# Kernel tuning notes

Hardware: AMD Instinct MI355X
Metric: run time of the kernel (lower is better)

Reference implementation:

```python
import jax, jax.numpy as jnp
import numpy as np

B, S, D, H = 2, 2048, 1024, 16
DH = D // H


def setup_inputs() -> dict:
    key = jax.random.key(0)
    ks = jax.random.split(key, 12)
    f = lambda k, sh: jax.random.normal(k, sh, dtype=jnp.float32)
    inp = {"q": f(ks[0], (B, S, D)), "k": f(ks[1], (B, S, D)), "v": f(ks[2], (B, S, D))}
    scale = 1.0 / np.sqrt(D)
    names = ["q", "k", "v", "o"]
    for i, n in enumerate(names):
        inp["W" + n] = f(ks[3 + i], (D, D)) * scale
        inp["b" + n] = f(ks[7 + i], (D,)) * scale
    # causal mask: True = masked out
    inp["mask"] = jnp.triu(jnp.ones((S, S), dtype=bool), k=1)[None, None]
    return inp


def _rope(x):
    # x: [b, h, s, dh]; non-standard RoPE from AbsPositionEncoding
    s, dh = x.shape[2], x.shape[3]
    inv = jnp.exp(jnp.arange(0, dh, 2, dtype=jnp.float32) * (-(4.0 * jnp.log(jnp.float32(10.0))) / dh))
    pos = jnp.arange(s, dtype=jnp.float32)[:, None]
    sin = jnp.sin(pos * inv)  # [s, dh/2]
    cos = jnp.cos(pos * inv)
    x1 = x[..., 0::2]
    x2 = x[..., 1::2]
    out = jnp.stack([x1 * sin - x2 * cos, -x1 * cos - x2 * sin], axis=-1)
    return out.reshape(x.shape)


def reference(q, k, v, Wq, bq, Wk, bk, Wv, bv, Wo, bo, mask):
    b, s, d = q.shape
    h, dh = H, DH

    def proj(x, W, bias):
        return (x @ W.T + bias).reshape(b, -1, h, dh).transpose(0, 2, 1, 3)

    Q = proj(q, Wq, bq)
    K = proj(k, Wk, bk)
    V = proj(v, Wv, bv)
    PQ = _rope(Q)
    PK = _rope(K)
    # NOTE: source's forward() path applies NO 1/sqrt(dh) scaling
    scores = jnp.einsum('bhqd,bhkd->bhqk', PQ, PK)
    neg = jnp.finfo(scores.dtype).min
    scores = jnp.where(mask, neg, scores)
    p = jax.nn.softmax(scores, axis=-1)
    p = jnp.where(mask, jnp.float32(0.0), p)
    out = jnp.einsum('bhqk,bhkd->bhqd', p, V)
    out = out.transpose(0, 2, 1, 3).reshape(b, s, d)
    return out @ Wo.T + bo
```

## Files before the change

kernel.cpp:

```cpp
#include <hip/hip_runtime.h>
#include <stdint.h>

#define BB 2
#define SS 2048
#define DD 1024
#define HH 16
#define DH 64
#define MM 4096
#define NQT 32

typedef __attribute__((ext_vector_type(8))) short short8;
typedef __attribute__((ext_vector_type(4))) float floatx4;
typedef unsigned short u16;

#define MFMA16(a,b,c) __builtin_amdgcn_mfma_f32_16x16x32_bf16((a),(b),(c),0,0,0)

__device__ __forceinline__ u16 f2bf(float f) {
  unsigned u = __float_as_uint(f);
  u += 0x7fffu + ((u >> 16) & 1u);
  return (u16)(u >> 16);
}

__device__ __forceinline__ void gll16(const void* g, void* l) {
  __builtin_amdgcn_global_load_lds((const __attribute__((address_space(1))) void*)g,
                                   (__attribute__((address_space(3))) void*)l,
                                   16, 0, 0);
}

__global__ __launch_bounds__(256) void sincos_k(float2* __restrict__ tab) {
  const int t = blockIdx.x * 256 + threadIdx.x;
  const int s = t >> 5, j = t & 31;
  const float inv = expf(-(float)j * (0.125f * 2.302585092994046f));
  const float a = (float)s * inv;
  tab[t] = make_float2(sinf(a), cosf(a));
}

__global__ __launch_bounds__(256) void conv_qkv(const float* __restrict__ a, const float* __restrict__ b,
                                                const float* __restrict__ c,
                                                u16* __restrict__ oa, u16* __restrict__ ob, u16* __restrict__ oc) {
  const float* s = blockIdx.y == 0 ? a : (blockIdx.y == 1 ? b : c);
  u16* d = blockIdx.y == 0 ? oa : (blockIdx.y == 1 ? ob : oc);
  const int i = (blockIdx.x * 256 + threadIdx.x) * 4;
  const float4 x = *(const float4*)(s + i);
  ushort4 p; p.x = f2bf(x.x); p.y = f2bf(x.y); p.z = f2bf(x.z); p.w = f2bf(x.w);
  *(ushort4*)(d + i) = p;
}

__global__ __launch_bounds__(256) void conv_w(const float* __restrict__ a, const float* __restrict__ b,
                                              const float* __restrict__ c, const float* __restrict__ d4,
                                              u16* __restrict__ oa, u16* __restrict__ ob,
                                              u16* __restrict__ oc, u16* __restrict__ od) {
  const float* s = blockIdx.y == 0 ? a : (blockIdx.y == 1 ? b : (blockIdx.y == 2 ? c : d4));
  u16* d = blockIdx.y == 0 ? oa : (blockIdx.y == 1 ? ob : (blockIdx.y == 2 ? oc : od));
  const int i = (blockIdx.x * 256 + threadIdx.x) * 4;
  const float4 x = *(const float4*)(s + i);
  ushort4 p; p.x = f2bf(x.x); p.y = f2bf(x.y); p.z = f2bf(x.z); p.w = f2bf(x.w);
  *(ushort4*)(d + i) = p;
}

__device__ __forceinline__ void gemm_body(const u16* __restrict__ A, const u16* __restrict__ Bt,
                                          const float* __restrict__ bias, float* __restrict__ C,
                                          int M, int N, int K, u16* As, u16* Bs) {
  const int tid = threadIdx.x;
  const int w = tid >> 6, l = tid & 63;
  const int lr = l & 15, lq = l >> 4;
  const int m0 = blockIdx.y * 128, n0 = blockIdx.x * 128;
  const int wm = (w >> 1) * 64, wn = (w & 1) * 64;

  floatx4 acc[4][4];
#pragma unroll
  for (int i = 0; i < 4; ++i)
#pragma unroll
    for (int j = 0; j < 4; ++j) acc[i][j] = (floatx4){0.f, 0.f, 0.f, 0.f};

  const int srow = w * 32 + (l >> 2);
  const int scol = (l & 3) * 8;
  const u16* ag = A + (size_t)(m0 + srow) * K + scol;
  const u16* bg = Bt + (size_t)(n0 + srow) * K + scol;
  u16* as0 = &As[w * 1024];
  u16* bs0 = &Bs[w * 1024];

  for (int k0 = 0; k0 < K; k0 += 32) {
    gll16(ag + k0, as0);
    gll16(ag + (size_t)16 * K + k0, as0 + 512);
    gll16(bg + k0, bs0);
    gll16(bg + (size_t)16 * K + k0, bs0 + 512);
    __syncthreads();
    short8 af[4], bfv[4];
#pragma unroll
    for (int i = 0; i < 4; ++i) af[i] = *(const short8*)&As[(wm + i * 16 + lr) * 32 + lq * 8];
#pragma unroll
    for (int j = 0; j < 4; ++j) bfv[j] = *(const short8*)&Bs[(wn + j * 16 + lr) * 32 + lq * 8];
    __builtin_amdgcn_s_setprio(1);
#pragma unroll
    for (int i = 0; i < 4; ++i)
#pragma unroll
      for (int j = 0; j < 4; ++j) acc[i][j] = MFMA16(af[i], bfv[j], acc[i][j]);
    __builtin_amdgcn_s_setprio(0);
    __syncthreads();
  }

#pragma unroll
  for (int i = 0; i < 4; ++i) {
    const int row = m0 + wm + i * 16 + lq * 4;
#pragma unroll
    for (int j = 0; j < 4; ++j) {
      const int col = n0 + wn + j * 16 + lr;
      const float bv = bias[col];
      float* cp = C + (size_t)row * N + col;
#pragma unroll
      for (int r = 0; r < 4; ++r) cp[(size_t)r * N] = acc[i][j][r] + bv;
    }
  }
}

__global__ __launch_bounds__(256) void gemm_bt(const u16* __restrict__ A, const u16* __restrict__ Bt,
                                               const float* __restrict__ bias, float* __restrict__ C,
                                               int M, int N, int K) {
  __shared__ alignas(16) u16 As[128 * 32];
  __shared__ alignas(16) u16 Bs[128 * 32];
  gemm_body(A, Bt, bias, C, M, N, K, As, Bs);
}

__global__ __launch_bounds__(256) void gemm3(const u16* __restrict__ A0, const u16* __restrict__ A1, const u16* __restrict__ A2,
                                             const u16* __restrict__ B0, const u16* __restrict__ B1, const u16* __restrict__ B2,
                                             const float* __restrict__ c0, const float* __restrict__ c1, const float* __restrict__ c2,
                                             float* __restrict__ C0, float* __restrict__ C1, float* __restrict__ C2) {
  __shared__ alignas(16) u16 As[128 * 32];
  __shared__ alignas(16) u16 Bs[128 * 32];
  const int z = blockIdx.z;
  const u16* A = z == 0 ? A0 : (z == 1 ? A1 : A2);
  const u16* Bt = z == 0 ? B0 : (z == 1 ? B1 : B2);
  const float* bias = z == 0 ? c0 : (z == 1 ? c1 : c2);
  float* C = z == 0 ? C0 : (z == 1 ? C1 : C2);
  gemm_body(A, Bt, bias, C, MM, DD, DD, As, Bs);
}

__global__ __launch_bounds__(256) void rope_post(const float* __restrict__ Qlin, const float* __restrict__ Klin,
                                                 const float2* __restrict__ tab,
                                                 u16* __restrict__ Qo, u16* __restrict__ Ko) {
  const int t = blockIdx.x * 256 + threadIdx.x;
  const int j = t & 31;
  const int h = (t >> 5) & 15;
  const int row = t >> 9;
  const int s = row & (SS - 1);
  const int b = row >> 11;
  const float* src = blockIdx.z ? Klin : Qlin;
  u16* dst = blockIdx.z ? Ko : Qo;
  const float2 x = *(const float2*)(src + (size_t)row * DD + h * 64 + 2 * j);
  const float2 sc = tab[s * 32 + j];
  const float e = x.x * sc.x - x.y * sc.y;
  const float o = -x.x * sc.y - x.y * sc.x;
  const size_t oi = ((size_t)(b * HH + h) * SS + s) * DH + 2 * j;
  ushort2 pk; pk.x = f2bf(e); pk.y = f2bf(o);
  *(ushort2*)(dst + oi) = pk;
}

__global__ __launch_bounds__(256) void v_post(const float* __restrict__ Vlin, u16* __restrict__ Vt) {
  __shared__ alignas(16) u16 tile[64][72];
  const int s0 = blockIdx.x * 64;
  const int bh = blockIdx.y;
  const int b = bh >> 4, h = bh & 15;
  const int t = threadIdx.x;
  const int sr = t >> 4;
  const int e4 = (t & 15) * 4;
#pragma unroll
  for (int it = 0; it < 4; ++it) {
    const int srow = sr + it * 16;
    const float4 x = *(const float4*)(Vlin + ((size_t)(b * SS + s0 + srow)) * DD + h * 64 + e4);
    tile[e4 + 0][srow] = f2bf(x.x);
    tile[e4 + 1][srow] = f2bf(x.y);
    tile[e4 + 2][srow] = f2bf(x.z);
    tile[e4 + 3][srow] = f2bf(x.w);
  }
  __syncthreads();
  const int e = t >> 2;
  const int sc = (t & 3) * 16;
  u16* op = Vt + ((size_t)bh * DH + e) * SS + s0 + sc;
  *(short8*)op = *(const short8*)&tile[e][sc];
  *(short8*)(op + 8) = *(const short8*)&tile[e][sc + 8];
}

__global__ __launch_bounds__(256) void attn_fwd(const u16* __restrict__ Qr, const u16* __restrict__ Kr,
                                                const u16* __restrict__ Vt, u16* __restrict__ O) {
  __shared__ alignas(16) u16 Ks[2][64 * 64];
  __shared__ alignas(16) u16 Vs[2][64 * 64];
  __shared__ alignas(16) u16 P[4][16][72];
  const int bid = blockIdx.x;
  const int qt = (NQT - 1) - (bid >> 5);
  const int bh = bid & 31;
  const int w = threadIdx.x >> 6, l = threadIdx.x & 63;
  const int lr = l & 15, lq = l >> 4;
  const int q0 = qt * 64 + w * 16;
  const u16* Qh = Qr + (size_t)bh * SS * DH;
  const u16* Kh = Kr + (size_t)bh * SS * DH;
  const u16* Vh = Vt + (size_t)bh * DH * SS;

  const short8 qf0 = *(const short8*)(Qh + (size_t)(q0 + lr) * DH + lq * 8);
  const short8 qf1 = *(const short8*)(Qh + (size_t)(q0 + lr) * DH + 32 + lq * 8);

  const int srow = w * 16 + (l >> 3);
  const int scolb = (l & 7) * 16;
  const int sgofs = ((scolb ^ (((l >> 3) & 7) << 4)) >> 1);

  floatx4 oacc[4];
#pragma unroll
  for (int n = 0; n < 4; ++n) oacc[n] = (floatx4){0.f, 0.f, 0.f, 0.f};
  float mrun[4] = {-1e30f, -1e30f, -1e30f, -1e30f};
  float lrun[4] = {0.f, 0.f, 0.f, 0.f};

  const int swz = (lr & 7) << 4;

#define STAGE(buf, kv0)                                                                  \
  do {                                                                                   \
    gll16(Kh + (size_t)((kv0) + srow) * DH + sgofs,       &Ks[buf][(w * 16) * 64]);      \
    gll16(Kh + (size_t)((kv0) + srow + 8) * DH + sgofs,   &Ks[buf][(w * 16 + 8) * 64]);  \
    gll16(Vh + (size_t)srow * SS + (kv0) + sgofs,         &Vs[buf][(w * 16) * 64]);      \
    gll16(Vh + (size_t)(srow + 8) * SS + (kv0) + sgofs,   &Vs[buf][(w * 16 + 8) * 64]);  \
  } while (0)

  STAGE(0, 0);
  __syncthreads();

  for (int t = 0; t <= qt; ++t) {
    const int cur = t & 1;
    if (t < qt) STAGE(cur ^ 1, (t + 1) * 64);
    const int kv0 = t * 64;

    floatx4 s[4];
    __builtin_amdgcn_s_setprio(1);
#pragma unroll
    for (int t4 = 0; t4 < 4; ++t4) {
      const int krow = t4 * 16 + lr;
      floatx4 z = (floatx4){0.f, 0.f, 0.f, 0.f};
      z = MFMA16(qf0, *(const short8*)&Ks[cur][krow * 64 + (((lq * 16) ^ swz) >> 1)], z);
      z = MFMA16(qf1, *(const short8*)&Ks[cur][krow * 64 + (((64 + lq * 16) ^ swz) >> 1)], z);
      s[t4] = z;
    }
    __builtin_amdgcn_s_setprio(0);

    if (t == qt) {
#pragma unroll
      for (int t4 = 0; t4 < 4; ++t4) {
        const int kcol = kv0 + t4 * 16 + lr;
#pragma unroll
        for (int r = 0; r < 4; ++r)
          if (kcol > q0 + lq * 4 + r) s[t4][r] = -1e30f;
      }
    }

    float scale[4];
#pragma unroll
    for (int r = 0; r < 4; ++r) {
      float mx = fmaxf(fmaxf(s[0][r], s[1][r]), fmaxf(s[2][r], s[3][r]));
      mx = fmaxf(mx, __shfl_xor(mx, 1));
      mx = fmaxf(mx, __shfl_xor(mx, 2));
      mx = fmaxf(mx, __shfl_xor(mx, 4));
      mx = fmaxf(mx, __shfl_xor(mx, 8));
      const float mn = fmaxf(mrun[r], mx);
      scale[r] = __expf(mrun[r] - mn);
      mrun[r] = mn;
      float rs = 0.f;
#pragma unroll
      for (int t4 = 0; t4 < 4; ++t4) {
        const float p = __expf(s[t4][r] - mn);
        s[t4][r] = p;
        rs += p;
      }
      rs += __shfl_xor(rs, 1);
      rs += __shfl_xor(rs, 2);
      rs += __shfl_xor(rs, 4);
      rs += __shfl_xor(rs, 8);
      lrun[r] = lrun[r] * scale[r] + rs;
    }
    const floatx4 sv = {scale[0], scale[1], scale[2], scale[3]};
#pragma unroll
    for (int n = 0; n < 4; ++n) oacc[n] *= sv;
#pragma unroll
    for (int t4 = 0; t4 < 4; ++t4)
#pragma unroll
      for (int r = 0; r < 4; ++r)
        P[w][lq * 4 + r][t4 * 16 + lr] = f2bf(s[t4][r]);

    __builtin_amdgcn_s_setprio(1);
#pragma unroll
    for (int kk = 0; kk < 2; ++kk) {
      const short8 pf = *(const short8*)&P[w][lr][kk * 32 + lq * 8];
#pragma unroll
      for (int n = 0; n < 4; ++n) {
        const int vrow = n * 16 + lr;
        oacc[n] = MFMA16(pf, *(const short8*)&Vs[cur][vrow * 64 + (((kk * 64 + lq * 16) ^ swz) >> 1)], oacc[n]);
      }
    }
    __builtin_amdgcn_s_setprio(0);
    __syncthreads();
  }
#undef STAGE

  const int b = bh >> 4, h = bh & 15;
#pragma unroll
  for (int n = 0; n < 4; ++n)
#pragma unroll
    for (int r = 0; r < 4; ++r) {
      const int qrow = q0 + lq * 4 + r;
      const float ov = oacc[n][r] / lrun[r];
      O[((size_t)(b * SS + qrow)) * DD + h * DH + n * 16 + lr] = f2bf(ov);
    }
}

extern "C" void kernel_launch(void* const* d_in, const int* in_sizes, int n_in,
                              void* d_out, int out_size, void* d_ws, size_t ws_size,
                              hipStream_t stream) {
  (void)in_sizes; (void)n_in; (void)out_size; (void)ws_size;
  const float* q  = (const float*)d_in[0];
  const float* k  = (const float*)d_in[1];
  const float* v  = (const float*)d_in[2];
  const float* Wq = (const float*)d_in[3];
  const float* bq = (const float*)d_in[4];
  const float* Wk = (const float*)d_in[5];
  const float* bk = (const float*)d_in[6];
  const float* Wv = (const float*)d_in[7];
  const float* bv = (const float*)d_in[8];
  const float* Wo = (const float*)d_in[9];
  const float* bo = (const float*)d_in[10];
  float* out = (float*)d_out;

  char* ws = (char*)d_ws;
  size_t off = 0;
  auto carve = [&](size_t bytes) { char* p = ws + off; off += (bytes + 255) & ~(size_t)255; return p; };
  u16* qb   = (u16*)carve((size_t)MM * DD * 2);
  u16* kb   = (u16*)carve((size_t)MM * DD * 2);
  u16* vb   = (u16*)carve((size_t)MM * DD * 2);
  u16* wqb  = (u16*)carve((size_t)DD * DD * 2);
  u16* wkb  = (u16*)carve((size_t)DD * DD * 2);
  u16* wvb  = (u16*)carve((size_t)DD * DD * 2);
  u16* wob  = (u16*)carve((size_t)DD * DD * 2);
  float* Qlin = (float*)carve((size_t)MM * DD * 4);
  float* Klin = (float*)carve((size_t)MM * DD * 4);
  float* Vlin = (float*)carve((size_t)MM * DD * 4);
  u16* Vtr  = (u16*)carve((size_t)MM * DD * 2);
  float2* tab = (float2*)carve((size_t)SS * 32 * 8);
  u16* Qro = qb;
  u16* Kro = kb;
  u16* Ob  = vb;

  sincos_k<<<SS * 32 / 256, 256, 0, stream>>>(tab);
  conv_qkv<<<dim3(MM * DD / 1024, 3), 256, 0, stream>>>(q, k, v, qb, kb, vb);
  conv_w<<<dim3(DD * DD / 1024, 4), 256, 0, stream>>>(Wq, Wk, Wv, Wo, wqb, wkb, wvb, wob);
  gemm3<<<dim3(DD / 128, MM / 128, 3), 256, 0, stream>>>(qb, kb, vb, wqb, wkb, wvb,
                                                         bq, bk, bv, Qlin, Klin, Vlin);
  rope_post<<<dim3(MM * DD / 2 / 256, 1, 2), 256, 0, stream>>>(Qlin, Klin, tab, Qro, Kro);
  v_post<<<dim3(SS / 64, BB * HH), 256, 0, stream>>>(Vlin, Vtr);
  attn_fwd<<<NQT * BB * HH, 256, 0, stream>>>(Qro, Kro, Vtr, Ob);
  gemm_bt<<<dim3(DD / 128, MM / 128), 256, 0, stream>>>(Ob, wob, bo, out, MM, DD, DD);
}
```

Baseline: 287.9 us.

## Rewrite attention with 32x32 MFMA, 128-row query tiles and register-resident P

The attention kernel now uses 32x32x16 bf16 MFMAs and computes transposed scores (K as A operand), so each lane owns a single query row. Each block covers 128 query rows, 32 per wave, instead of 64, and per-wave causal skipping is added. The probability matrix is packed to bf16 with v_cvt_pk and exchanged across half-waves with shuffles instead of a round trip through LDS. This cuts LDS traffic and the cross-lane reductions in the softmax, but halves the block count (512 blocks) and raises register pressure.

```diff
diff --git a/kernel.cpp b/kernel.cpp
--- a/kernel.cpp
+++ b/kernel.cpp
@@ -7,18 +7,26 @@
 #define HH 16
 #define DH 64
 #define MM 4096
-#define NQT 32
+#define NQTB 16
 
 typedef __attribute__((ext_vector_type(8))) short short8;
 typedef __attribute__((ext_vector_type(4))) float floatx4;
+typedef __attribute__((ext_vector_type(16))) float floatx16;
 typedef unsigned short u16;
 
 #define MFMA16(a,b,c) __builtin_amdgcn_mfma_f32_16x16x32_bf16((a),(b),(c),0,0,0)
+#define MFMA32(a,b,c) __builtin_amdgcn_mfma_f32_32x32x16_bf16((a),(b),(c),0,0,0)
 
 __device__ __forceinline__ u16 f2bf(float f) {
   unsigned u = __float_as_uint(f);
   u += 0x7fffu + ((u >> 16) & 1u);
   return (u16)(u >> 16);
+}
+
+__device__ __forceinline__ unsigned cvtpk(float lo, float hi2) {
+  unsigned r;
+  asm("v_cvt_pk_bf16_f32 %0, %1, %2" : "=v"(r) : "v"(lo), "v"(hi2));
+  return r;
 }
 
 __device__ __forceinline__ void gll16(const void* g, void* l) {
@@ -185,31 +193,31 @@
                                                 const u16* __restrict__ Vt, u16* __restrict__ O) {
   __shared__ alignas(16) u16 Ks[2][64 * 64];
   __shared__ alignas(16) u16 Vs[2][64 * 64];
-  __shared__ alignas(16) u16 P[4][16][72];
   const int bid = blockIdx.x;
-  const int qt = (NQT - 1) - (bid >> 5);
+  const int qt = (NQTB - 1) - (bid >> 5);
   const int bh = bid & 31;
   const int w = threadIdx.x >> 6, l = threadIdx.x & 63;
-  const int lr = l & 15, lq = l >> 4;
-  const int q0 = qt * 64 + w * 16;
+  const int ql = l & 31, hi = l >> 5;
+  const int qw0 = qt * 128 + w * 32;
   const u16* Qh = Qr + (size_t)bh * SS * DH;
   const u16* Kh = Kr + (size_t)bh * SS * DH;
   const u16* Vh = Vt + (size_t)bh * DH * SS;
 
-  const short8 qf0 = *(const short8*)(Qh + (size_t)(q0 + lr) * DH + lq * 8);
-  const short8 qf1 = *(const short8*)(Qh + (size_t)(q0 + lr) * DH + 32 + lq * 8);
+  short8 qf[4];
+#pragma unroll
+  for (int i = 0; i < 4; ++i)
+    qf[i] = *(const short8*)(Qh + (size_t)(qw0 + ql) * DH + i * 16 + hi * 8);
+
+  floatx16 oacc[2];
+#pragma unroll
+  for (int dt = 0; dt < 2; ++dt)
+#pragma unroll
+    for (int r = 0; r < 16; ++r) oacc[dt][r] = 0.f;
+  float mrun = -1e30f, lrun = 0.f;
 
   const int srow = w * 16 + (l >> 3);
-  const int scolb = (l & 7) * 16;
-  const int sgofs = ((scolb ^ (((l >> 3) & 7) << 4)) >> 1);
-
-  floatx4 oacc[4];
-#pragma unroll
-  for (int n = 0; n < 4; ++n) oacc[n] = (floatx4){0.f, 0.f, 0.f, 0.f};
-  float mrun[4] = {-1e30f, -1e30f, -1e30f, -1e30f};
-  float lrun[4] = {0.f, 0.f, 0.f, 0.f};
-
-  const int swz = (lr & 7) << 4;
+  const int sgofs = ((((l & 7) * 16) ^ (((l >> 3) & 7) << 4)) >> 1);
+  const int swzb = (ql & 7) << 4;
 
 #define STAGE(buf, kv0)                                                                  \
   do {                                                                                   \
@@ -219,92 +227,118 @@
     gll16(Vh + (size_t)(srow + 8) * SS + (kv0) + sgofs,   &Vs[buf][(w * 16 + 8) * 64]);  \
   } while (0)
 
+  const int T = 2 * qt + 2;
   STAGE(0, 0);
   __syncthreads();
 
-  for (int t = 0; t <= qt; ++t) {
+  for (int t = 0; t < T; ++t) {
     const int cur = t & 1;
-    if (t < qt) STAGE(cur ^ 1, (t + 1) * 64);
+    if (t < T - 1) STAGE(cur ^ 1, (t + 1) * 64);
     const int kv0 = t * 64;
 
-    floatx4 s[4];
-    __builtin_amdgcn_s_setprio(1);
-#pragma unroll
-    for (int t4 = 0; t4 < 4; ++t4) {
-      const int krow = t4 * 16 + lr;
-      floatx4 z = (floatx4){0.f, 0.f, 0.f, 0.f};
-      z = MFMA16(qf0, *(const short8*)&Ks[cur][krow * 64 + (((lq * 16) ^ swz) >> 1)], z);
-      z = MFMA16(qf1, *(const short8*)&Ks[cur][krow * 64 + (((64 + lq * 16) ^ swz) >> 1)], z);
-      s[t4] = z;
+    if (kv0 <= qw0 + 31) {
+      floatx16 st[2];
+#pragma unroll
+      for (int tt = 0; tt < 2; ++tt)
+#pragma unroll
+        for (int r = 0; r < 16; ++r) st[tt][r] = 0.f;
+      __builtin_amdgcn_s_setprio(1);
+#pragma unroll
+      for (int tt = 0; tt < 2; ++tt)
+#pragma unroll
+        for (int i = 0; i < 4; ++i) {
+          const u16* kp = &Ks[cur][(tt * 32 + ql) * 64 + (((32 * i + 16 * hi) ^ swzb) >> 1)];
+          st[tt] = MFMA32(*(const short8*)kp, qf[i], st[tt]);
+        }
+      __builtin_amdgcn_s_setprio(0);
+
+      if (kv0 + 63 > qw0) {
+#pragma unroll
+        for (int tt = 0; tt < 2; ++tt)
+#pragma unroll
+          for (int r = 0; r < 16; ++r) {
+            const int kv = kv0 + tt * 32 + (r & 3) + 8 * (r >> 2) + 4 * hi;
+            if (kv > qw0 + ql) st[tt][r] = -1e30f;
+          }
+      }
+
+      floatx16 mx;
+#pragma unroll
+      for (int r = 0; r < 16; ++r) mx[r] = fmaxf(st[0][r], st[1][r]);
+      float m8[8];
+#pragma unroll
+      for (int r = 0; r < 8; ++r) m8[r] = fmaxf(mx[r], mx[r + 8]);
+      float m4a = fmaxf(m8[0], m8[4]), m4b = fmaxf(m8[1], m8[5]);
+      float m4c = fmaxf(m8[2], m8[6]), m4d = fmaxf(m8[3], m8[7]);
+      float tmax = fmaxf(fmaxf(m4a, m4b), fmaxf(m4c, m4d));
+      tmax = fmaxf(tmax, __shfl_xor(tmax, 32));
+      const float mn = fmaxf(mrun, tmax);
+      const float sc = __expf(mrun - mn);
+      mrun = mn;
+      float ps = 0.f;
+#pragma unroll
+      for (int tt = 0; tt < 2; ++tt)
+#pragma unroll
+        for (int r = 0; r < 16; ++r) {
+          const float p = __expf(st[tt][r] - mn);
+          st[tt][r] = p;
+          ps += p;
+        }
+      ps += __shfl_xor(ps, 32);
+      lrun = lrun * sc + ps;
+#pragma unroll
+      for (int dt = 0; dt < 2; ++dt)
+#pragma unroll
+        for (int r = 0; r < 16; ++r) oacc[dt][r] *= sc;
+
+      short8 pfrag[4];
+#pragma unroll
+      for (int c = 0; c < 4; ++c) {
+        const int tt = c >> 1;
+        const int A0 = 2 * (c & 1), A1 = A0 + 1;
+        const unsigned P00 = cvtpk(st[tt][4 * A0 + 0], st[tt][4 * A0 + 1]);
+        const unsigned P01 = cvtpk(st[tt][4 * A0 + 2], st[tt][4 * A0 + 3]);
+        const unsigned P10 = cvtpk(st[tt][4 * A1 + 0], st[tt][4 * A1 + 1]);
+        const unsigned P11 = cvtpk(st[tt][4 * A1 + 2], st[tt][4 * A1 + 3]);
+        const unsigned S0 = hi ? P00 : P10;
+        const unsigned S1 = hi ? P01 : P11;
+        const unsigned R0 = (unsigned)__shfl_xor((int)S0, 32);
+        const unsigned R1 = (unsigned)__shfl_xor((int)S1, 32);
+        union { unsigned u[4]; short8 s; } fd;
+        fd.u[0] = hi ? R0 : P00;
+        fd.u[1] = hi ? R1 : P01;
+        fd.u[2] = hi ? P10 : R0;
+        fd.u[3] = hi ? P11 : R1;
+        pfrag[c] = fd.s;
+      }
+
+      __builtin_amdgcn_s_setprio(1);
+#pragma unroll
+      for (int dt = 0; dt < 2; ++dt)
+#pragma unroll
+        for (int c = 0; c < 4; ++c) {
+          const u16* vp = &Vs[cur][(dt * 32 + ql) * 64 + (((32 * c + 16 * hi) ^ swzb) >> 1)];
+          oacc[dt] = MFMA32(*(const short8*)vp, pfrag[c], oacc[dt]);
+        }
+      __builtin_amdgcn_s_setprio(0);
     }
-    __builtin_amdgcn_s_setprio(0);
-
-    if (t == qt) {
-#pragma unroll
-      for (int t4 = 0; t4 < 4; ++t4) {
-        const int kcol = kv0 + t4 * 16 + lr;
-#pragma unroll
-        for (int r = 0; r < 4; ++r)
-          if (kcol > q0 + lq * 4 + r) s[t4][r] = -1e30f;
-      }
-    }
-
-    float scale[4];
-#pragma unroll
-    for (int r = 0; r < 4; ++r) {
-      float mx = fmaxf(fmaxf(s[0][r], s[1][r]), fmaxf(s[2][r], s[3][r]));
-      mx = fmaxf(mx, __shfl_xor(mx, 1));
-      mx = fmaxf(mx, __shfl_xor(mx, 2));
-      mx = fmaxf(mx, __shfl_xor(mx, 4));
-      mx = fmaxf(mx, __shfl_xor(mx, 8));
-      const float mn = fmaxf(mrun[r], mx);
-      scale[r] = __expf(mrun[r] - mn);
-      mrun[r] = mn;
-      float rs = 0.f;
-#pragma unroll
-      for (int t4 = 0; t4 < 4; ++t4) {
-        const float p = __expf(s[t4][r] - mn);
-        s[t4][r] = p;
-        rs += p;
-      }
-      rs += __shfl_xor(rs, 1);
-      rs += __shfl_xor(rs, 2);
-      rs += __shfl_xor(rs, 4);
-      rs += __shfl_xor(rs, 8);
-      lrun[r] = lrun[r] * scale[r] + rs;
-    }
-    const floatx4 sv = {scale[0], scale[1], scale[2], scale[3]};
-#pragma unroll
-    for (int n = 0; n < 4; ++n) oacc[n] *= sv;
-#pragma unroll
-    for (int t4 = 0; t4 < 4; ++t4)
-#pragma unroll
-      for (int r = 0; r < 4; ++r)
-        P[w][lq * 4 + r][t4 * 16 + lr] = f2bf(s[t4][r]);
-
-    __builtin_amdgcn_s_setprio(1);
-#pragma unroll
-    for (int kk = 0; kk < 2; ++kk) {
-      const short8 pf = *(const short8*)&P[w][lr][kk * 32 + lq * 8];
-#pragma unroll
-      for (int n = 0; n < 4; ++n) {
-        const int vrow = n * 16 + lr;
-        oacc[n] = MFMA16(pf, *(const short8*)&Vs[cur][vrow * 64 + (((kk * 64 + lq * 16) ^ swz) >> 1)], oacc[n]);
-      }
-    }
-    __builtin_amdgcn_s_setprio(0);
     __syncthreads();
   }
 #undef STAGE
 
+  const float inv = 1.0f / lrun;
   const int b = bh >> 4, h = bh & 15;
-#pragma unroll
-  for (int n = 0; n < 4; ++n)
-#pragma unroll
-    for (int r = 0; r < 4; ++r) {
-      const int qrow = q0 + lq * 4 + r;
-      const float ov = oacc[n][r] / lrun[r];
-      O[((size_t)(b * SS + qrow)) * DD + h * DH + n * 16 + lr] = f2bf(ov);
+  u16* orow = O + ((size_t)(b * SS + qw0 + ql)) * DD + h * DH;
+#pragma unroll
+  for (int dt = 0; dt < 2; ++dt)
+#pragma unroll
+    for (int g = 0; g < 4; ++g) {
+      ushort4 pk;
+      pk.x = f2bf(oacc[dt][4 * g + 0] * inv);
+      pk.y = f2bf(oacc[dt][4 * g + 1] * inv);
+      pk.z = f2bf(oacc[dt][4 * g + 2] * inv);
+      pk.w = f2bf(oacc[dt][4 * g + 3] * inv);
+      *(ushort4*)(orow + dt * 32 + 8 * g + 4 * hi) = pk;
     }
 }
 
@@ -351,6 +385,6 @@
                                                          bq, bk, bv, Qlin, Klin, Vlin);
   rope_post<<<dim3(MM * DD / 2 / 256, 1, 2), 256, 0, stream>>>(Qlin, Klin, tab, Qro, Kro);
   v_post<<<dim3(SS / 64, BB * HH), 256, 0, stream>>>(Vlin, Vtr);
-  attn_fwd<<<NQT * BB * HH, 256, 0, stream>>>(Qro, Kro, Vtr, Ob);
+  attn_fwd<<<NQTB * BB * HH, 256, 0, stream>>>(Qro, Kro, Vtr, Ob);
   gemm_bt<<<dim3(DD / 128, MM / 128), 256, 0, stream>>>(Ob, wob, bo, out, MM, DD, DD);
 }
```

Result: faster. 278.7 us (-3.2%).
